# Performance work log

Measured on AMD Instinct MI355X. Metric: run time of the kernel, lower is better.

Reference implementation:

```python
import jax, jax.numpy as jnp
import numpy as np

DIMS, K_SIZE, V_SIZE, SEQ_LEN = 1024, 128, 128, 2048
MINUS = -100.0


def setup_inputs() -> dict:
    key = jax.random.key(0)
    k1, k2, k3, k4, k5 = jax.random.split(key, 5)
    B, S = 8, 2048
    minibatch = jax.random.normal(k1, (B, S, DIMS), dtype=jnp.float32)
    # Linear params (torch nn.Linear default init scale ~ U(-1/sqrt(fan_in), ...)); use scaled normals
    s = 1.0 / np.sqrt(DIMS)
    Wk = jax.random.normal(k2, (DIMS, K_SIZE), dtype=jnp.float32) * s
    bk = jax.random.normal(k3, (K_SIZE,), dtype=jnp.float32) * s
    Wv = jax.random.normal(k4, (DIMS, V_SIZE), dtype=jnp.float32) * s
    bv = jax.random.normal(k5, (V_SIZE,), dtype=jnp.float32) * s
    return {"minibatch": minibatch, "Wk": Wk, "bk": bk, "Wv": Wv, "bv": bv,
            "current_seq_len": S}


def reference(minibatch, Wk, bk, Wv, bv, current_seq_len):
    # keys == queries (shared projection, as in the original forward)
    keys = minibatch @ Wk + bk              # [B,S,K]
    values = minibatch @ Wv + bv            # [B,S,V]
    S = current_seq_len
    mask = jnp.tril(jnp.ones((S, S), dtype=jnp.float32))  # [S,S] lower-triangular
    scores = jnp.einsum('bsk,btk->bst', keys, keys) / np.sqrt(K_SIZE)
    logits = mask * scores + MINUS * (1.0 - mask)
    probs = jax.nn.softmax(logits, axis=2)
    read = jnp.einsum('bst,btv->bsv', probs, values)  # [B,S,V]
    return jnp.concatenate([minibatch, read], axis=2)  # [B,S,dims+V]
```

## Files before the change

### kernel.cpp

```cpp
#include <hip/hip_runtime.h>
#include <hip/hip_bf16.h>

#define BATCH 8
#define SEQ   2048
#define DMS   1024
#define KSZ   128
#define OD    1152

typedef unsigned short u16;
typedef unsigned int   u32;
typedef __attribute__((ext_vector_type(4)))  float  f32x4;
typedef __attribute__((ext_vector_type(16))) float  f32x16;
typedef __attribute__((ext_vector_type(8)))  __bf16 bf16x8;

union U128 { uint4 u4; bf16x8 b8; u16 us[8]; u32 u[4]; };

__device__ inline u16 f2bf(float f) {
  union { __bf16 h; u16 u; } c;
  c.h = (__bf16)f;
  return c.u;
}

__device__ inline float fexp2(float x) {
  float r;
  asm("v_exp_f32 %0, %1" : "=v"(r) : "v"(x));
  return r;
}

__device__ inline f32x4 mfma16(bf16x8 a, bf16x8 b, f32x4 c) {
  return __builtin_amdgcn_mfma_f32_16x16x32_bf16(a, b, c, 0, 0, 0);
}
__device__ inline f32x16 mfma32(bf16x8 a, bf16x8 b, f32x16 c) {
  return __builtin_amdgcn_mfma_f32_32x32x16_bf16(a, b, c, 0, 0, 0);
}

__device__ inline uint4 pack8bf(float4 a, float4 b) {
  U128 w;
  w.us[0] = f2bf(a.x); w.us[1] = f2bf(a.y);
  w.us[2] = f2bf(a.z); w.us[3] = f2bf(a.w);
  w.us[4] = f2bf(b.x); w.us[5] = f2bf(b.y);
  w.us[6] = f2bf(b.z); w.us[7] = f2bf(b.w);
  return w.u4;
}

__device__ inline void glds16(const u16* src, u16* ldsDst) {
  __builtin_amdgcn_global_load_lds(
      (const __attribute__((address_space(1))) u32*)src,
      (__attribute__((address_space(3))) u32*)ldsDst, 16, 0, 0);
}

#define BSTRIDE 262144

__global__ void __launch_bounds__(256) prep_kernel(
    const float* __restrict__ Wk, const float* __restrict__ Wv,
    u16* __restrict__ Wtiles)
{
  int T = blockIdx.x * 256 + threadIdx.x;
  int n  = T & 255;
  int kc = (T >> 8) * 8;
  int ks = kc >> 6;
  int kk = kc & 63;
  const float* src = (n < 128) ? (Wk + n) : (Wv + (n - 128));
  U128 w;
#pragma unroll
  for (int j = 0; j < 8; ++j) w.us[j] = f2bf(src[(size_t)(kc + j) * KSZ]);
  u16* dst = Wtiles + ks * 16384 + n * 64 + (kk ^ ((n & 7) << 3));
  *(uint4*)dst = w.u4;
}

__global__ void __launch_bounds__(256, 2) proj_kernel(
    const float* __restrict__ X, const u16* __restrict__ Wtiles,
    const float* __restrict__ bk, const float* __restrict__ bv,
    u16* __restrict__ Kfrag, u16* __restrict__ Vfrag)
{
  __shared__ u16 Ab[2][32 * 64];
  __shared__ u16 Bt[2][256 * 64];

  const int tid  = threadIdx.x;
  const int lane = tid & 63;
  const int wid  = tid >> 6;
  const int l15  = lane & 15;
  const int g    = lane >> 4;
  const int m0   = blockIdx.x * 32;

  const int ar = tid >> 3;
  const int ac = (tid & 7) * 8;

  const float* xrow  = X + (size_t)(m0 + ar) * DMS + ac;
  const int    abOff = (ar * 128 + ac * 2) ^ ((ar & 7) << 4);

  char* AbB = (char*)&Ab[0][0];
  char* BtB = (char*)&Bt[0][0];

  f32x4 acc[2][4];
#pragma unroll
  for (int i = 0; i < 2; ++i)
#pragma unroll
    for (int j = 0; j < 4; ++j) acc[i][j] = (f32x4){0.f, 0.f, 0.f, 0.f};

  float4 xv[2][2];

  xv[0][0] = *(const float4*)(xrow);
  xv[0][1] = *(const float4*)(xrow + 4);
  {
    const u16* ws = Wtiles + wid * 4096 + lane * 8;
    u16* wd = &Bt[0][0] + wid * 4096;
#pragma unroll
    for (int r = 0; r < 8; ++r) glds16(ws + r * 512, wd + r * 512);
  }
  *(uint4*)(AbB + abOff) = pack8bf(xv[0][0], xv[0][1]);
  __syncthreads();

#pragma unroll
  for (int k = 0; k < 16; ++k) {
    const int cur = k & 1, nxt = cur ^ 1;
    if (k < 15) {
      xv[nxt][0] = *(const float4*)(xrow + (k + 1) * 64);
      xv[nxt][1] = *(const float4*)(xrow + (k + 1) * 64 + 4);
      const u16* ws = Wtiles + (size_t)(k + 1) * 16384 + wid * 4096 + lane * 8;
      u16* wd = &Bt[nxt][0] + wid * 4096;
#pragma unroll
      for (int r = 0; r < 8; ++r) glds16(ws + r * 512, wd + r * 512);
    }
#pragma unroll
    for (int kh = 0; kh < 2; ++kh) {
      bf16x8 af[2], bfr[4];
#pragma unroll
      for (int mf = 0; mf < 2; ++mf) {
        int m = mf * 16 + l15;
        int ab = cur * 4096 + ((m * 128 + (kh * 32 + g * 8) * 2) ^ ((m & 7) << 4));
        U128 u; u.u4 = *(uint4*)(AbB + ab); af[mf] = u.b8;
      }
#pragma unroll
      for (int nf = 0; nf < 4; ++nf) {
        int n = wid * 64 + nf * 16 + l15;
        int bb = cur * 32768 + ((n * 128 + (kh * 32 + g * 8) * 2) ^ ((n & 7) << 4));
        U128 u; u.u4 = *(uint4*)(BtB + bb); bfr[nf] = u.b8;
      }
#pragma unroll
      for (int mf = 0; mf < 2; ++mf)
#pragma unroll
        for (int nf = 0; nf < 4; ++nf)
          acc[mf][nf] = mfma16(af[mf], bfr[nf], acc[mf][nf]);
    }
    if (k < 15)
      *(uint4*)(AbB + nxt * 4096 + abOff) = pack8bf(xv[nxt][0], xv[nxt][1]);
    __syncthreads();
  }

  u16* Ct = &Bt[0][0];
#pragma unroll
  for (int nf = 0; nf < 4; ++nf) {
    int n = wid * 64 + nf * 16 + l15;
    float bias = (n < 128) ? bk[n] : bv[n - 128];
#pragma unroll
    for (int mf = 0; mf < 2; ++mf)
#pragma unroll
      for (int j = 0; j < 4; ++j) {
        int s = mf * 16 + g * 4 + j;
        Ct[s * 256 + (n ^ ((s & 7) << 3))] = f2bf(acc[mf][nf][j] + bias);
      }
  }
  __syncthreads();

  const int bb   = m0 >> 11;
  const int tloc = (m0 & 2047) >> 5;

  {
    int sl = tid >> 3;
    int ks = tid & 7;
    u16* dst = Kfrag + (size_t)bb * BSTRIDE + (size_t)(tloc * 8 + ks) * 512 + sl * 8;
#pragma unroll
    for (int hi2 = 0; hi2 < 2; ++hi2) {
      int n = ks * 16 + hi2 * 8;
      uint4 v = *(const uint4*)&Ct[sl * 256 + (n ^ ((sl & 7) << 3))];
      *(uint4*)(dst + hi2 * 256) = v;
    }
  }
  {
    int l31 = tid & 31;
    int vb2 = (tid >> 5) & 3;
    int th  = tid >> 7;
    int n   = 128 + vb2 * 32 + l31;
    u16* dst = Vfrag + (size_t)bb * BSTRIDE +
               (size_t)((tloc * 4 + vb2) * 2 + th) * 512 + l31 * 8;
#pragma unroll
    for (int hi = 0; hi < 2; ++hi) {
      U128 w;
#pragma unroll
      for (int j = 0; j < 8; ++j) {
        int s = th * 16 + hi * 8 + j;
        w.us[j] = Ct[s * 256 + (n ^ ((s & 7) << 3))];
      }
      *(uint4*)(dst + hi * 256) = w.u4;
    }
  }
}

__global__ void __launch_bounds__(256, 2) attn_kernel(
    const u16* __restrict__ Kfrag, const u16* __restrict__ Vfrag,
    const float* __restrict__ X, float* __restrict__ out)
{
  __shared__ float Om[4][128][33];
  __shared__ float Ml[4][2][32];
  __shared__ float Wm[4][32];
  __shared__ float Li[32];

  const int tid  = threadIdx.x;
  const int lane = tid & 63;
  const int w    = tid >> 6;
  const int l31  = lane & 31;
  const int hi   = lane >> 5;

  const int bi = blockIdx.x;
  const int b  = bi & 7;
  const int qt = (bi < 256) ? (63 - (bi >> 3)) : ((bi >> 3) - 32);
  const int q0 = qt * 32;

  const u16* Kb = Kfrag + (size_t)b * BSTRIDE;
  const u16* Vb = Vfrag + (size_t)b * BSTRIDE;
  const int loff = hi * 256 + l31 * 8;

  bf16x8 qf[8];
  {
    const u16* qp = Kb + (size_t)(qt * 8) * 512 + loff;
#pragma unroll
    for (int ks = 0; ks < 8; ++ks) {
      U128 u; u.u4 = *(const uint4*)(qp + ks * 512); qf[ks] = u.b8;
    }
  }

  f32x16 o[4];
#pragma unroll
  for (int vb2 = 0; vb2 < 4; ++vb2)
#pragma unroll
    for (int i = 0; i < 16; ++i) o[vb2][i] = 0.f;

  float mrun = -3.0e38f, lsum = 0.f;
  const float SC  = 0.08838834764831845f;
  const float L2E = 1.44269504088896341f;

  bf16x8 kf[8];
  {
    int ti0 = (w <= qt) ? w : 0;
    const u16* kp = Kb + (size_t)(ti0 * 8) * 512 + loff;
#pragma unroll
    for (int ks = 0; ks < 8; ++ks) {
      U128 u; u.u4 = *(const uint4*)(kp + ks * 512); kf[ks] = u.b8;
    }
  }

  for (int ti = w; ti <= qt; ti += 4) {
    bf16x8 vf[4][2];
    {
      const u16* vp = Vb + (size_t)(ti * 8) * 512 + loff;
#pragma unroll
      for (int vb2 = 0; vb2 < 4; ++vb2)
#pragma unroll
        for (int th = 0; th < 2; ++th) {
          U128 u; u.u4 = *(const uint4*)(vp + (vb2 * 2 + th) * 512);
          vf[vb2][th] = u.b8;
        }
    }
    f32x16 s;
#pragma unroll
    for (int i = 0; i < 16; ++i) s[i] = 0.f;
#pragma unroll
    for (int ks = 0; ks < 8; ++ks) s = mfma32(kf[ks], qf[ks], s);
    {
      int tin = (ti + 4 <= qt) ? ti + 4 : ti;
      const u16* kp = Kb + (size_t)(tin * 8) * 512 + loff;
#pragma unroll
      for (int ks = 0; ks < 8; ++ks) {
        U128 u; u.u4 = *(const uint4*)(kp + ks * 512); kf[ks] = u.b8;
      }
    }
    float sv[16];
#pragma unroll
    for (int r = 0; r < 16; ++r) sv[r] = s[r] * SC;
    if (ti == qt) {
#pragma unroll
      for (int r = 0; r < 16; ++r) {
        int toff = (r & 3) + 8 * (r >> 2) + 4 * hi;
        if (toff > l31) sv[r] = -3.0e38f;
      }
    }
    float mx = sv[0];
#pragma unroll
    for (int r = 1; r < 16; ++r) mx = fmaxf(mx, sv[r]);
    mx = fmaxf(mx, __shfl_xor(mx, 32));
    float p[16];
    float ps = 0.f;
    if (__all(mx - mrun <= 8.0f)) {
#pragma unroll
      for (int r = 0; r < 16; ++r) { p[r] = fexp2((sv[r] - mrun) * L2E); ps += p[r]; }
      ps += __shfl_xor(ps, 32);
      lsum += ps;
    } else {
      float mnew = fmaxf(mrun, mx);
      float al = fexp2((mrun - mnew) * L2E);
#pragma unroll
      for (int r = 0; r < 16; ++r) { p[r] = fexp2((sv[r] - mnew) * L2E); ps += p[r]; }
      ps += __shfl_xor(ps, 32);
      lsum = lsum * al + ps;
      mrun = mnew;
#pragma unroll
      for (int vb2 = 0; vb2 < 4; ++vb2)
#pragma unroll
        for (int i = 0; i < 16; ++i) o[vb2][i] *= al;
    }
    u32 c01 = (u32)f2bf(p[0])  | ((u32)f2bf(p[1])  << 16);
    u32 c23 = (u32)f2bf(p[2])  | ((u32)f2bf(p[3])  << 16);
    u32 c45 = (u32)f2bf(p[4])  | ((u32)f2bf(p[5])  << 16);
    u32 c67 = (u32)f2bf(p[6])  | ((u32)f2bf(p[7])  << 16);
    u32 c89 = (u32)f2bf(p[8])  | ((u32)f2bf(p[9])  << 16);
    u32 cAB = (u32)f2bf(p[10]) | ((u32)f2bf(p[11]) << 16);
    u32 cCD = (u32)f2bf(p[12]) | ((u32)f2bf(p[13]) << 16);
    u32 cEF = (u32)f2bf(p[14]) | ((u32)f2bf(p[15]) << 16);
    u32 d01 = __shfl_xor(c01, 32);
    u32 d23 = __shfl_xor(c23, 32);
    u32 d45 = __shfl_xor(c45, 32);
    u32 d67 = __shfl_xor(c67, 32);
    u32 d89 = __shfl_xor(c89, 32);
    u32 dAB = __shfl_xor(cAB, 32);
    u32 dCD = __shfl_xor(cCD, 32);
    u32 dEF = __shfl_xor(cEF, 32);
    U128 pf1, pf2;
    pf1.u[0] = hi ? d45 : c01;
    pf1.u[1] = hi ? d67 : c23;
    pf1.u[2] = hi ? c45 : d01;
    pf1.u[3] = hi ? c67 : d23;
    pf2.u[0] = hi ? dCD : c89;
    pf2.u[1] = hi ? dEF : cAB;
    pf2.u[2] = hi ? cCD : d89;
    pf2.u[3] = hi ? cEF : dAB;
#pragma unroll
    for (int vb2 = 0; vb2 < 4; ++vb2) {
      o[vb2] = mfma32(vf[vb2][0], pf1.b8, o[vb2]);
      o[vb2] = mfma32(vf[vb2][1], pf2.b8, o[vb2]);
    }
  }

#pragma unroll
  for (int vb2 = 0; vb2 < 4; ++vb2)
#pragma unroll
    for (int r = 0; r < 16; ++r) {
      int v = vb2 * 32 + (r & 3) + 8 * (r >> 2) + 4 * hi;
      Om[w][v][l31] = o[vb2][r];
    }
  if (lane < 32) {
    Ml[w][0][l31] = mrun;
    Ml[w][1][l31] = lsum;
  }
  __syncthreads();

  if (tid < 32) {
    float m0 = Ml[0][0][tid], m1 = Ml[1][0][tid];
    float m2 = Ml[2][0][tid], m3 = Ml[3][0][tid];
    float M  = fmaxf(fmaxf(m0, m1), fmaxf(m2, m3));
    float w0 = fexp2((m0 - M) * L2E), w1 = fexp2((m1 - M) * L2E);
    float w2 = fexp2((m2 - M) * L2E), w3 = fexp2((m3 - M) * L2E);
    float L  = Ml[0][1][tid] * w0 + Ml[1][1][tid] * w1 +
               Ml[2][1][tid] * w2 + Ml[3][1][tid] * w3;
    Wm[0][tid] = w0; Wm[1][tid] = w1; Wm[2][tid] = w2; Wm[3][tid] = w3;
    Li[tid] = 1.f / L;
  }
  __syncthreads();

  {
    const int q = tid >> 3;
    const int vbase = (tid & 7) * 16;
    float wq0 = Wm[0][q], wq1 = Wm[1][q], wq2 = Wm[2][q], wq3 = Wm[3][q];
    float li = Li[q];
    float* orow = out + (size_t)(b * SEQ + q0 + q) * OD + 1024 + vbase;
#pragma unroll
    for (int i = 0; i < 16; i += 4) {
      float4 res;
      res.x = (Om[0][vbase + i + 0][q] * wq0 + Om[1][vbase + i + 0][q] * wq1 +
               Om[2][vbase + i + 0][q] * wq2 + Om[3][vbase + i + 0][q] * wq3) * li;
      res.y = (Om[0][vbase + i + 1][q] * wq0 + Om[1][vbase + i + 1][q] * wq1 +
               Om[2][vbase + i + 1][q] * wq2 + Om[3][vbase + i + 1][q] * wq3) * li;
      res.z = (Om[0][vbase + i + 2][q] * wq0 + Om[1][vbase + i + 2][q] * wq1 +
               Om[2][vbase + i + 2][q] * wq2 + Om[3][vbase + i + 2][q] * wq3) * li;
      res.w = (Om[0][vbase + i + 3][q] * wq0 + Om[1][vbase + i + 3][q] * wq1 +
               Om[2][vbase + i + 3][q] * wq2 + Om[3][vbase + i + 3][q] * wq3) * li;
      *(float4*)(orow + i) = res;
    }
  }

  {
#pragma unroll
    for (int r0 = 0; r0 < 32; r0 += 8) {
      float4 t[8];
#pragma unroll
      for (int j = 0; j < 8; ++j)
        t[j] = *((const float4*)(X + (size_t)(b * SEQ + q0 + r0 + j) * DMS) + tid);
#pragma unroll
      for (int j = 0; j < 8; ++j)
        *((float4*)(out + (size_t)(b * SEQ + q0 + r0 + j) * OD) + tid) = t[j];
    }
  }
}

extern "C" void kernel_launch(void* const* d_in, const int* in_sizes, int n_in,
                              void* d_out, int out_size, void* d_ws, size_t ws_size,
                              hipStream_t stream)
{
  const float* X  = (const float*)d_in[0];
  const float* Wk = (const float*)d_in[1];
  const float* bk = (const float*)d_in[2];
  const float* Wv = (const float*)d_in[3];
  const float* bv = (const float*)d_in[4];
  float* out = (float*)d_out;

  u16* Kfrag  = (u16*)d_ws;
  u16* Vfrag  = Kfrag + (size_t)BATCH * BSTRIDE;
  u16* Wtiles = Vfrag + (size_t)BATCH * BSTRIDE;

  prep_kernel<<<dim3(128), dim3(256), 0, stream>>>(Wk, Wv, Wtiles);
  proj_kernel<<<dim3(512), dim3(256), 0, stream>>>(X, Wtiles, bk, bv, Kfrag, Vfrag);
  attn_kernel<<<dim3(512), dim3(256), 0, stream>>>(Kfrag, Vfrag, X, out);
}
```

Measured before the change: 69.22 us.

## Pre-convert X to swizzled bf16 tiles and split projection GEMM by K/V halves

Adds a separate kernel that converts the fp32 input to bf16 in pre-swizzled 64x64 tiles, so the projection GEMM can stream both operands with asynchronous global-to-LDS loads. The GEMM now uses 64-row by 128-column tiles, with each block computing either the key or the value half. This removes register staging and in-loop packing, but adds a full extra write and re-read of a bf16 copy of X plus one more kernel launch. It also needs extra workspace.

```diff
diff --git a/kernel.cpp b/kernel.cpp
--- a/kernel.cpp
+++ b/kernel.cpp
@@ -60,139 +60,157 @@
   int kc = (T >> 8) * 8;
   int ks = kc >> 6;
   int kk = kc & 63;
-  const float* src = (n < 128) ? (Wk + n) : (Wv + (n - 128));
+  int nh = n >> 7;
+  int n1 = n & 127;
+  const float* src = nh ? (Wv + n1) : (Wk + n1);
   U128 w;
 #pragma unroll
   for (int j = 0; j < 8; ++j) w.us[j] = f2bf(src[(size_t)(kc + j) * KSZ]);
-  u16* dst = Wtiles + ks * 16384 + n * 64 + (kk ^ ((n & 7) << 3));
+  u16* dst = Wtiles + ks * 16384 + nh * 8192 + n1 * 64 + (kk ^ ((n1 & 7) << 3));
   *(uint4*)dst = w.u4;
 }
 
-__global__ void __launch_bounds__(256, 2) proj_kernel(
-    const float* __restrict__ X, const u16* __restrict__ Wtiles,
+__global__ void __launch_bounds__(256) cvt_kernel(
+    const float* __restrict__ X, u16* __restrict__ Xtiles)
+{
+  int T = blockIdx.x * 256 + threadIdx.x;
+  int row = T >> 7;
+  int c   = T & 127;
+  const float4* xp = (const float4*)(X + (size_t)row * DMS + c * 8);
+  float4 a0 = xp[0], a1 = xp[1];
+  int rt = row >> 6, r = row & 63, ks = c >> 3, kk0 = (c & 7) * 8;
+  u16* dst = Xtiles + (size_t)(rt * 16 + ks) * 4096 + r * 64 + (kk0 ^ ((r & 7) << 3));
+  *(uint4*)dst = pack8bf(a0, a1);
+}
+
+__global__ void __launch_bounds__(256, 3) gemm_kernel(
+    const u16* __restrict__ Xtiles, const u16* __restrict__ Wtiles,
     const float* __restrict__ bk, const float* __restrict__ bv,
     u16* __restrict__ Kfrag, u16* __restrict__ Vfrag)
 {
-  __shared__ u16 Ab[2][32 * 64];
-  __shared__ u16 Bt[2][256 * 64];
+  __shared__ u16 Ab[2][64 * 64];
+  __shared__ u16 Bt[2][128 * 64];
 
   const int tid  = threadIdx.x;
   const int lane = tid & 63;
-  const int wid  = tid >> 6;
+  const int w    = tid >> 6;
   const int l15  = lane & 15;
   const int g    = lane >> 4;
-  const int m0   = blockIdx.x * 32;
-
-  const int ar = tid >> 3;
-  const int ac = (tid & 7) * 8;
-
-  const float* xrow  = X + (size_t)(m0 + ar) * DMS + ac;
-  const int    abOff = (ar * 128 + ac * 2) ^ ((ar & 7) << 4);
-
+
+  const int bi = blockIdx.x;
+  const int nh = bi & 1;
+  const int rt = bi >> 1;
+
+  const u16* abase = Xtiles + (size_t)rt * 16 * 4096;
+  const u16* wbase = Wtiles + nh * 8192;
   char* AbB = (char*)&Ab[0][0];
   char* BtB = (char*)&Bt[0][0];
 
-  f32x4 acc[2][4];
-#pragma unroll
-  for (int i = 0; i < 2; ++i)
-#pragma unroll
-    for (int j = 0; j < 4; ++j) acc[i][j] = (f32x4){0.f, 0.f, 0.f, 0.f};
-
-  float4 xv[2][2];
-
-  xv[0][0] = *(const float4*)(xrow);
-  xv[0][1] = *(const float4*)(xrow + 4);
-  {
-    const u16* ws = Wtiles + wid * 4096 + lane * 8;
-    u16* wd = &Bt[0][0] + wid * 4096;
-#pragma unroll
-    for (int r = 0; r < 8; ++r) glds16(ws + r * 512, wd + r * 512);
-  }
-  *(uint4*)(AbB + abOff) = pack8bf(xv[0][0], xv[0][1]);
+  f32x4 acc[4][2];
+#pragma unroll
+  for (int i = 0; i < 4; ++i)
+#pragma unroll
+    for (int j = 0; j < 2; ++j) acc[i][j] = (f32x4){0.f, 0.f, 0.f, 0.f};
+
+#define STAGE(K, BUF)                                                          \
+  {                                                                            \
+    const u16* as = abase + (size_t)(K) * 4096;                                \
+    u16* ad = &Ab[BUF][0];                                                     \
+    _Pragma("unroll")                                                          \
+    for (int i = 0; i < 2; ++i)                                                \
+      glds16(as + (w * 2 + i) * 512 + lane * 8, ad + (w * 2 + i) * 512);       \
+    const u16* ws = wbase + (size_t)(K) * 16384;                               \
+    u16* wd = &Bt[BUF][0];                                                     \
+    _Pragma("unroll")                                                          \
+    for (int i = 0; i < 4; ++i)                                                \
+      glds16(ws + (w * 4 + i) * 512 + lane * 8, wd + (w * 4 + i) * 512);       \
+  }
+
+  STAGE(0, 0)
   __syncthreads();
 
 #pragma unroll
   for (int k = 0; k < 16; ++k) {
     const int cur = k & 1, nxt = cur ^ 1;
-    if (k < 15) {
-      xv[nxt][0] = *(const float4*)(xrow + (k + 1) * 64);
-      xv[nxt][1] = *(const float4*)(xrow + (k + 1) * 64 + 4);
-      const u16* ws = Wtiles + (size_t)(k + 1) * 16384 + wid * 4096 + lane * 8;
-      u16* wd = &Bt[nxt][0] + wid * 4096;
-#pragma unroll
-      for (int r = 0; r < 8; ++r) glds16(ws + r * 512, wd + r * 512);
-    }
+    if (k < 15) STAGE(k + 1, nxt)
 #pragma unroll
     for (int kh = 0; kh < 2; ++kh) {
-      bf16x8 af[2], bfr[4];
-#pragma unroll
-      for (int mf = 0; mf < 2; ++mf) {
+      bf16x8 af[4], bfr[2];
+#pragma unroll
+      for (int mf = 0; mf < 4; ++mf) {
         int m = mf * 16 + l15;
-        int ab = cur * 4096 + ((m * 128 + (kh * 32 + g * 8) * 2) ^ ((m & 7) << 4));
-        U128 u; u.u4 = *(uint4*)(AbB + ab); af[mf] = u.b8;
-      }
-#pragma unroll
-      for (int nf = 0; nf < 4; ++nf) {
-        int n = wid * 64 + nf * 16 + l15;
-        int bb = cur * 32768 + ((n * 128 + (kh * 32 + g * 8) * 2) ^ ((n & 7) << 4));
-        U128 u; u.u4 = *(uint4*)(BtB + bb); bfr[nf] = u.b8;
-      }
-#pragma unroll
-      for (int mf = 0; mf < 2; ++mf)
-#pragma unroll
-        for (int nf = 0; nf < 4; ++nf)
+        int idx = m * 64 + ((kh * 32 + g * 8) ^ ((m & 7) << 3));
+        U128 u; u.u4 = *(uint4*)(AbB + cur * 8192 + idx * 2); af[mf] = u.b8;
+      }
+#pragma unroll
+      for (int nf = 0; nf < 2; ++nf) {
+        int n1 = w * 32 + nf * 16 + l15;
+        int idx = n1 * 64 + ((kh * 32 + g * 8) ^ ((n1 & 7) << 3));
+        U128 u; u.u4 = *(uint4*)(BtB + cur * 16384 + idx * 2); bfr[nf] = u.b8;
+      }
+#pragma unroll
+      for (int mf = 0; mf < 4; ++mf)
+#pragma unroll
+        for (int nf = 0; nf < 2; ++nf)
           acc[mf][nf] = mfma16(af[mf], bfr[nf], acc[mf][nf]);
     }
-    if (k < 15)
-      *(uint4*)(AbB + nxt * 4096 + abOff) = pack8bf(xv[nxt][0], xv[nxt][1]);
     __syncthreads();
   }
-
+#undef STAGE
+
+  const float* bias_src = nh ? bv : bk;
   u16* Ct = &Bt[0][0];
 #pragma unroll
-  for (int nf = 0; nf < 4; ++nf) {
-    int n = wid * 64 + nf * 16 + l15;
-    float bias = (n < 128) ? bk[n] : bv[n - 128];
-#pragma unroll
-    for (int mf = 0; mf < 2; ++mf)
+  for (int nf = 0; nf < 2; ++nf) {
+    int n1 = w * 32 + nf * 16 + l15;
+    float bs = bias_src[n1];
+#pragma unroll
+    for (int mf = 0; mf < 4; ++mf)
 #pragma unroll
       for (int j = 0; j < 4; ++j) {
         int s = mf * 16 + g * 4 + j;
-        Ct[s * 256 + (n ^ ((s & 7) << 3))] = f2bf(acc[mf][nf][j] + bias);
+        Ct[s * 128 + (n1 ^ ((s & 7) << 3))] = f2bf(acc[mf][nf][j] + bs);
       }
   }
   __syncthreads();
 
-  const int bb   = m0 >> 11;
-  const int tloc = (m0 & 2047) >> 5;
-
-  {
-    int sl = tid >> 3;
-    int ks = tid & 7;
-    u16* dst = Kfrag + (size_t)bb * BSTRIDE + (size_t)(tloc * 8 + ks) * 512 + sl * 8;
-#pragma unroll
-    for (int hi2 = 0; hi2 < 2; ++hi2) {
-      int n = ks * 16 + hi2 * 8;
-      uint4 v = *(const uint4*)&Ct[sl * 256 + (n ^ ((sl & 7) << 3))];
-      *(uint4*)(dst + hi2 * 256) = v;
-    }
-  }
-  {
+  const int bb   = rt >> 5;
+  const int tloc = (rt & 31) * 2;
+
+  if (nh == 0) {
+#pragma unroll
+    for (int p = 0; p < 2; ++p) {
+      int s   = (tid >> 3) + p * 32;
+      int ks2 = tid & 7;
+      int t2  = tloc + (s >> 5);
+      int l31 = s & 31;
+      u16* dst = Kfrag + (size_t)bb * BSTRIDE + (size_t)(t2 * 8 + ks2) * 512 + l31 * 8;
+#pragma unroll
+      for (int hi2 = 0; hi2 < 2; ++hi2) {
+        int n1 = ks2 * 16 + hi2 * 8;
+        uint4 v = *(const uint4*)&Ct[s * 128 + (n1 ^ ((s & 7) << 3))];
+        *(uint4*)(dst + hi2 * 256) = v;
+      }
+    }
+  } else {
     int l31 = tid & 31;
     int vb2 = (tid >> 5) & 3;
     int th  = tid >> 7;
-    int n   = 128 + vb2 * 32 + l31;
-    u16* dst = Vfrag + (size_t)bb * BSTRIDE +
-               (size_t)((tloc * 4 + vb2) * 2 + th) * 512 + l31 * 8;
-#pragma unroll
-    for (int hi = 0; hi < 2; ++hi) {
-      U128 w;
-#pragma unroll
-      for (int j = 0; j < 8; ++j) {
-        int s = th * 16 + hi * 8 + j;
-        w.us[j] = Ct[s * 256 + (n ^ ((s & 7) << 3))];
-      }
-      *(uint4*)(dst + hi * 256) = w.u4;
+#pragma unroll
+    for (int p = 0; p < 2; ++p) {
+      int t2 = tloc + p;
+#pragma unroll
+      for (int hi = 0; hi < 2; ++hi) {
+        U128 wv;
+#pragma unroll
+        for (int j = 0; j < 8; ++j) {
+          int s = p * 32 + th * 16 + hi * 8 + j;
+          wv.us[j] = Ct[s * 128 + ((vb2 * 32 + l31) ^ ((s & 7) << 3))];
+        }
+        u16* dst = Vfrag + (size_t)bb * BSTRIDE +
+                   (size_t)((t2 * 4 + vb2) * 2 + th) * 512 + hi * 256 + l31 * 8;
+        *(uint4*)dst = wv.u4;
+      }
     }
   }
 }
@@ -416,8 +434,10 @@
   u16* Kfrag  = (u16*)d_ws;
   u16* Vfrag  = Kfrag + (size_t)BATCH * BSTRIDE;
   u16* Wtiles = Vfrag + (size_t)BATCH * BSTRIDE;
+  u16* Xtiles = Wtiles + (size_t)262144;
 
   prep_kernel<<<dim3(128), dim3(256), 0, stream>>>(Wk, Wv, Wtiles);
-  proj_kernel<<<dim3(512), dim3(256), 0, stream>>>(X, Wtiles, bk, bv, Kfrag, Vfrag);
+  cvt_kernel<<<dim3(8192), dim3(256), 0, stream>>>(X, Xtiles);
+  gemm_kernel<<<dim3(512), dim3(256), 0, stream>>>(Xtiles, Wtiles, bk, bv, Kfrag, Vfrag);
   attn_kernel<<<dim3(512), dim3(256), 0, stream>>>(Kfrag, Vfrag, X, out);
 }
```

Result: slower. 78.26 us (+13.0%).

## Restructure projection GEMM with 64-row tiles and 128-wide weight slabs

Applied to the files above, without the earlier changes.

The projection GEMM now processes 64 rows per block (256 blocks instead of 512). Each wave loads its A fragment straight from global memory into registers instead of staging it in LDS, and the weights move in 128-deep K slabs of 64KB with single buffering. The aim is to halve total weight traffic into LDS and drop the A-tile LDS round trip. In exchange it loses the double-buffered overlap, since each slab load is bracketed by syncs. It also drops occupancy to one block per CU, which on a 256-CU part may leave some CUs idle.

```diff
diff --git a/kernel.cpp b/kernel.cpp
--- a/kernel.cpp
+++ b/kernel.cpp
@@ -53,113 +53,80 @@
 
 __global__ void __launch_bounds__(256) prep_kernel(
     const float* __restrict__ Wk, const float* __restrict__ Wv,
-    u16* __restrict__ Wtiles)
+    u16* __restrict__ Wslabs)
 {
   int T = blockIdx.x * 256 + threadIdx.x;
   int n  = T & 255;
   int kc = (T >> 8) * 8;
-  int ks = kc >> 6;
-  int kk = kc & 63;
+  int s  = kc >> 7;
+  int kk = kc & 127;
   const float* src = (n < 128) ? (Wk + n) : (Wv + (n - 128));
   U128 w;
 #pragma unroll
   for (int j = 0; j < 8; ++j) w.us[j] = f2bf(src[(size_t)(kc + j) * KSZ]);
-  u16* dst = Wtiles + ks * 16384 + n * 64 + (kk ^ ((n & 7) << 3));
+  u16* dst = Wslabs + s * 32768 + n * 128 + (kk ^ ((n & 7) << 3));
   *(uint4*)dst = w.u4;
 }
 
-__global__ void __launch_bounds__(256, 2) proj_kernel(
-    const float* __restrict__ X, const u16* __restrict__ Wtiles,
+__global__ void __launch_bounds__(256, 1) gemm_kernel(
+    const float* __restrict__ X, const u16* __restrict__ Wslabs,
     const float* __restrict__ bk, const float* __restrict__ bv,
     u16* __restrict__ Kfrag, u16* __restrict__ Vfrag)
 {
-  __shared__ u16 Ab[2][32 * 64];
-  __shared__ u16 Bt[2][256 * 64];
+  __shared__ u16 Ws[256 * 128];
 
   const int tid  = threadIdx.x;
   const int lane = tid & 63;
-  const int wid  = tid >> 6;
+  const int wv   = tid >> 6;
   const int l15  = lane & 15;
   const int g    = lane >> 4;
-  const int m0   = blockIdx.x * 32;
-
-  const int ar = tid >> 3;
-  const int ac = (tid & 7) * 8;
-
-  const float* xrow  = X + (size_t)(m0 + ar) * DMS + ac;
-  const int    abOff = (ar * 128 + ac * 2) ^ ((ar & 7) << 4);
-
-  char* AbB = (char*)&Ab[0][0];
-  char* BtB = (char*)&Bt[0][0];
-
-  f32x4 acc[2][4];
-#pragma unroll
-  for (int i = 0; i < 2; ++i)
-#pragma unroll
-    for (int j = 0; j < 4; ++j) acc[i][j] = (f32x4){0.f, 0.f, 0.f, 0.f};
-
-  float4 xv[2][2];
-
-  xv[0][0] = *(const float4*)(xrow);
-  xv[0][1] = *(const float4*)(xrow + 4);
-  {
-    const u16* ws = Wtiles + wid * 4096 + lane * 8;
-    u16* wd = &Bt[0][0] + wid * 4096;
-#pragma unroll
-    for (int r = 0; r < 8; ++r) glds16(ws + r * 512, wd + r * 512);
-  }
-  *(uint4*)(AbB + abOff) = pack8bf(xv[0][0], xv[0][1]);
+  const int m0   = blockIdx.x * 64;
+
+  const float* xrow = X + (size_t)(m0 + wv * 16 + l15) * DMS + g * 8;
+
+  f32x4 acc[16];
+#pragma unroll
+  for (int nf = 0; nf < 16; ++nf) acc[nf] = (f32x4){0.f, 0.f, 0.f, 0.f};
+
+#pragma unroll 1
+  for (int s = 0; s < 8; ++s) {
+    __syncthreads();
+    {
+      const u16* ws = Wslabs + s * 32768 + tid * 8;
+      u16* wd = Ws + tid * 8;
+#pragma unroll
+      for (int c = 0; c < 16; ++c) glds16(ws + c * 2048, wd + c * 2048);
+    }
+    float4 xv[8];
+#pragma unroll
+    for (int ks = 0; ks < 4; ++ks) {
+      xv[ks * 2]     = *(const float4*)(xrow + s * 128 + ks * 32);
+      xv[ks * 2 + 1] = *(const float4*)(xrow + s * 128 + ks * 32 + 4);
+    }
+    __syncthreads();
+#pragma unroll
+    for (int ks = 0; ks < 4; ++ks) {
+      U128 aw; aw.u4 = pack8bf(xv[ks * 2], xv[ks * 2 + 1]);
+#pragma unroll
+      for (int nf = 0; nf < 16; ++nf) {
+        int n = nf * 16 + l15;
+        int idx = n * 128 + ((ks * 32 + g * 8) ^ ((n & 7) << 3));
+        U128 u; u.u4 = *(const uint4*)(Ws + idx);
+        acc[nf] = mfma16(aw.b8, u.b8, acc[nf]);
+      }
+    }
+  }
+
   __syncthreads();
-
-#pragma unroll
-  for (int k = 0; k < 16; ++k) {
-    const int cur = k & 1, nxt = cur ^ 1;
-    if (k < 15) {
-      xv[nxt][0] = *(const float4*)(xrow + (k + 1) * 64);
-      xv[nxt][1] = *(const float4*)(xrow + (k + 1) * 64 + 4);
-      const u16* ws = Wtiles + (size_t)(k + 1) * 16384 + wid * 4096 + lane * 8;
-      u16* wd = &Bt[nxt][0] + wid * 4096;
-#pragma unroll
-      for (int r = 0; r < 8; ++r) glds16(ws + r * 512, wd + r * 512);
-    }
-#pragma unroll
-    for (int kh = 0; kh < 2; ++kh) {
-      bf16x8 af[2], bfr[4];
-#pragma unroll
-      for (int mf = 0; mf < 2; ++mf) {
-        int m = mf * 16 + l15;
-        int ab = cur * 4096 + ((m * 128 + (kh * 32 + g * 8) * 2) ^ ((m & 7) << 4));
-        U128 u; u.u4 = *(uint4*)(AbB + ab); af[mf] = u.b8;
-      }
-#pragma unroll
-      for (int nf = 0; nf < 4; ++nf) {
-        int n = wid * 64 + nf * 16 + l15;
-        int bb = cur * 32768 + ((n * 128 + (kh * 32 + g * 8) * 2) ^ ((n & 7) << 4));
-        U128 u; u.u4 = *(uint4*)(BtB + bb); bfr[nf] = u.b8;
-      }
-#pragma unroll
-      for (int mf = 0; mf < 2; ++mf)
-#pragma unroll
-        for (int nf = 0; nf < 4; ++nf)
-          acc[mf][nf] = mfma16(af[mf], bfr[nf], acc[mf][nf]);
-    }
-    if (k < 15)
-      *(uint4*)(AbB + nxt * 4096 + abOff) = pack8bf(xv[nxt][0], xv[nxt][1]);
-    __syncthreads();
-  }
-
-  u16* Ct = &Bt[0][0];
-#pragma unroll
-  for (int nf = 0; nf < 4; ++nf) {
-    int n = wid * 64 + nf * 16 + l15;
-    float bias = (n < 128) ? bk[n] : bv[n - 128];
-#pragma unroll
-    for (int mf = 0; mf < 2; ++mf)
-#pragma unroll
-      for (int j = 0; j < 4; ++j) {
-        int s = mf * 16 + g * 4 + j;
-        Ct[s * 256 + (n ^ ((s & 7) << 3))] = f2bf(acc[mf][nf][j] + bias);
-      }
+#pragma unroll
+  for (int nf = 0; nf < 16; ++nf) {
+    int n = nf * 16 + l15;
+    float bs = (n < 128) ? bk[n] : bv[n - 128];
+#pragma unroll
+    for (int j = 0; j < 4; ++j) {
+      int srow = wv * 16 + g * 4 + j;
+      Ws[srow * 256 + (n ^ ((srow & 7) << 3))] = f2bf(acc[nf][j] + bs);
+    }
   }
   __syncthreads();
 
@@ -167,32 +134,41 @@
   const int tloc = (m0 & 2047) >> 5;
 
   {
-    int sl = tid >> 3;
-    int ks = tid & 7;
-    u16* dst = Kfrag + (size_t)bb * BSTRIDE + (size_t)(tloc * 8 + ks) * 512 + sl * 8;
-#pragma unroll
-    for (int hi2 = 0; hi2 < 2; ++hi2) {
-      int n = ks * 16 + hi2 * 8;
-      uint4 v = *(const uint4*)&Ct[sl * 256 + (n ^ ((sl & 7) << 3))];
-      *(uint4*)(dst + hi2 * 256) = v;
+    int sl  = tid >> 2;
+    int t2  = tloc + (sl >> 5);
+    int l31 = sl & 31;
+#pragma unroll
+    for (int h = 0; h < 2; ++h) {
+      int ks2 = (tid & 3) * 2 + h;
+      u16* dst = Kfrag + (size_t)bb * BSTRIDE + (size_t)(t2 * 8 + ks2) * 512 + l31 * 8;
+#pragma unroll
+      for (int hi2 = 0; hi2 < 2; ++hi2) {
+        int n = ks2 * 16 + hi2 * 8;
+        uint4 v = *(const uint4*)&Ws[sl * 256 + (n ^ ((sl & 7) << 3))];
+        *(uint4*)(dst + hi2 * 256) = v;
+      }
     }
   }
   {
     int l31 = tid & 31;
     int vb2 = (tid >> 5) & 3;
-    int th  = tid >> 7;
+    int th  = (tid >> 7) & 1;
     int n   = 128 + vb2 * 32 + l31;
-    u16* dst = Vfrag + (size_t)bb * BSTRIDE +
-               (size_t)((tloc * 4 + vb2) * 2 + th) * 512 + l31 * 8;
-#pragma unroll
-    for (int hi = 0; hi < 2; ++hi) {
-      U128 w;
-#pragma unroll
-      for (int j = 0; j < 8; ++j) {
-        int s = th * 16 + hi * 8 + j;
-        w.us[j] = Ct[s * 256 + (n ^ ((s & 7) << 3))];
-      }
-      *(uint4*)(dst + hi * 256) = w.u4;
+#pragma unroll
+    for (int p = 0; p < 2; ++p) {
+      int t2 = tloc + p;
+#pragma unroll
+      for (int hi = 0; hi < 2; ++hi) {
+        U128 wvv;
+#pragma unroll
+        for (int j = 0; j < 8; ++j) {
+          int srow = p * 32 + th * 16 + hi * 8 + j;
+          wvv.us[j] = Ws[srow * 256 + (n ^ ((srow & 7) << 3))];
+        }
+        u16* dst = Vfrag + (size_t)bb * BSTRIDE +
+                   (size_t)((t2 * 4 + vb2) * 2 + th) * 512 + hi * 256 + l31 * 8;
+        *(uint4*)dst = wvv.u4;
+      }
     }
   }
 }
@@ -415,9 +391,9 @@
 
   u16* Kfrag  = (u16*)d_ws;
   u16* Vfrag  = Kfrag + (size_t)BATCH * BSTRIDE;
-  u16* Wtiles = Vfrag + (size_t)BATCH * BSTRIDE;
-
-  prep_kernel<<<dim3(128), dim3(256), 0, stream>>>(Wk, Wv, Wtiles);
-  proj_kernel<<<dim3(512), dim3(256), 0, stream>>>(X, Wtiles, bk, bv, Kfrag, Vfrag);
+  u16* Wslabs = Vfrag + (size_t)BATCH * BSTRIDE;
+
+  prep_kernel<<<dim3(128), dim3(256), 0, stream>>>(Wk, Wv, Wslabs);
+  gemm_kernel<<<dim3(256), dim3(256), 0, stream>>>(X, Wslabs, bk, bv, Kfrag, Vfrag);
   attn_kernel<<<dim3(512), dim3(256), 0, stream>>>(Kfrag, Vfrag, X, out);
 }
```

New measurement: 74.83 us. +8.1%, slower.
